# Kernel optimization log

Measured on AMD Instinct MI355X. Metric: run time of the kernel, lower is better.

The kernel has to match this reference:

```python
import jax, jax.numpy as jnp
import numpy as np

B, T, E, H = 32, 256, 1024, 1024


def setup_inputs() -> dict:
    key = jax.random.key(0)
    ks = jax.random.split(key, 8)
    stdv = 1.0 / np.sqrt(H)
    u = lambda k, shape: jax.random.uniform(k, shape, jnp.float32, -stdv, stdv)
    return {
        "x": jax.random.normal(ks[0], (B, T, E), jnp.float32),
        "mask": jnp.ones((B, T), jnp.float32),
        "W_ih0": u(ks[1], (E, 4 * H)),
        "W_hh0": u(ks[2], (H, 4 * H)),
        "b0": jnp.zeros((4 * H,), jnp.float32),
        "W_ih1": u(ks[3], (H, 4 * H)),
        "W_hh1": u(ks[4], (H, 4 * H)),
        "b1": jnp.zeros((4 * H,), jnp.float32),
    }


def _cell(inp, m_t, h0, c0, Wih, Whh, b):
    # pre-activations: [B, 4H]; gate order f, i, o, g (as in torch.split)
    pre = inp @ Wih + h0 @ Whh + b
    f, i, o, g = jnp.split(pre, 4, axis=1)
    m = m_t[:, None]
    c1 = jax.nn.sigmoid(f) * c0 + jax.nn.sigmoid(i) * jnp.tanh(g)
    c1 = c1 * m + c0 * (1.0 - m)
    h1 = jax.nn.sigmoid(o) * jnp.tanh(c1)
    h1 = h1 * m + h0 * (1.0 - m)
    return h1, c1


def reference(x, mask, W_ih0, W_hh0, b0, W_ih1, W_hh1, b1):
    Bz = x.shape[0]
    Hd = W_hh0.shape[0]

    def step(carry, xm):
        h0, c0, h1, c1 = carry
        xt, mt = xm
        # NOTE: layer 1 consumes PREVIOUS timestep's layer-0 hidden (source quirk)
        nh1, nc1 = _cell(h0, mt, h1, c1, W_ih1, W_hh1, b1)
        nh0, nc0 = _cell(xt, mt, h0, c0, W_ih0, W_hh0, b0)
        return (nh0, nc0, nh1, nc1), nh1

    z = jnp.zeros((Bz, Hd), x.dtype)
    init = (z, z, z, z)
    xs = (jnp.swapaxes(x, 0, 1), jnp.swapaxes(mask, 0, 1))  # [T,B,E], [T,B]
    _, hs = jax.lax.scan(step, init, xs)  # hs: [T, B, H]
    states = jnp.swapaxes(hs, 0, 1)  # [B, T, H]
    return states, mask
```

## Files before the change

kernel.cpp:

```cpp
#include <hip/hip_runtime.h>
#include <hip/hip_bf16.h>
#include <stdint.h>
#include <stddef.h>

#define TT    256
#define NBLK  128

typedef __attribute__((ext_vector_type(8))) short short8;
typedef __attribute__((ext_vector_type(4))) float f32x4;

__device__ __forceinline__ short f2bf(float v) {
  uint32_t u = __builtin_bit_cast(uint32_t, v);
  uint32_t r = (u + 0x7fffu + ((u >> 16) & 1u)) >> 16;
  return (short)r;
}

__device__ __forceinline__ void stage_coh(const short8* g, short8* l) {
  __builtin_amdgcn_global_load_lds(
      (const __attribute__((address_space(1))) void*)g,
      (__attribute__((address_space(3))) void*)l, 16, 0, 17);
}
__device__ __forceinline__ void stage_pln(const short8* g, short8* l) {
  __builtin_amdgcn_global_load_lds(
      (const __attribute__((address_space(1))) void*)g,
      (__attribute__((address_space(3))) void*)l, 16, 0, 0);
}

__global__ void k_init(const float* __restrict__ mask, float* __restrict__ out,
                       uint32_t* __restrict__ z) {
  int tid = blockIdx.x * blockDim.x + threadIdx.x;
  if (tid < 8192) out[8388608 + tid] = mask[tid];
  for (int j = tid; j < 51200; j += 16384) z[j] = 0;
}

__global__ void k_packw(const float* __restrict__ Wih0, const float* __restrict__ Whh0,
                        const float* __restrict__ Wih1, const float* __restrict__ Whh1,
                        short* __restrict__ Bp) {
  int cid = blockIdx.x * blockDim.x + threadIdx.x;
  int l    = cid & 63;
  int f    = (cid >> 6) & 63;
  int wgid = cid >> 12;
  int q  = l >> 4, cc = l & 15;
  int cg = f >> 4, s = f & 15;
  int w    = wgid & 3;
  int blk  = (wgid >> 2) & 63;
  bool p1  = (wgid >= 256);
  int precol = (cc >> 2) * 1024 + blk * 16 + cg * 4 + (cc & 3);
  const float* MA = p1 ? Wih1 : Wih0;
  const float* MB = p1 ? Whh1 : Whh0;
  short8 o;
#pragma unroll
  for (int j = 0; j < 8; ++j) {
    int k = w * 512 + s * 32 + q * 8 + j;
    const float* M = (k < 1024) ? MA : MB;
    o[j] = f2bf(M[(size_t)(k & 1023) * 4096 + precol]);
  }
  ((short8*)Bp)[cid] = o;
}

__global__ void k_packx(const float* __restrict__ x, short* __restrict__ Xb) {
  int tid = blockIdx.x * blockDim.x + threadIdx.x;
  int eg = tid & 127;
  int t  = (tid >> 7) & 255;
  int b  = tid >> 15;
  const float* src = x + ((size_t)(b * 256 + t) * 1024 + eg * 8);
  short8 o;
#pragma unroll
  for (int j = 0; j < 8; ++j) o[j] = f2bf(src[j]);
  ((short8*)Xb)[(t * 128 + eg) * 32 + b] = o;
}

__global__ __launch_bounds__(256, 1) void k_lstm(
    const float* __restrict__ mask, const float* __restrict__ b0,
    const float* __restrict__ b1,   const short* __restrict__ Bp,
    const short* __restrict__ Xb,   short* __restrict__ h0r,
    short* __restrict__ h1b,        float* __restrict__ out,
    uint32_t* bar) {
  __shared__ short8 stg[8192];
  f32x4 (*xch)[4][2][64] = (f32x4 (*)[4][2][64])(void*)stg;
  short* hstage = (short*)(void*)(stg + 2048);

  const int tid  = threadIdx.x;
  const int wv   = tid >> 6;
  const int lane = tid & 63;
  const int quad = lane >> 4;
  const int cc   = lane & 15;
  const int bid  = blockIdx.x;
  const bool is1 = (bid >= 64);
  const int blk  = bid & 63;
  const int wgid = (is1 ? 256 : 0) + blk * 4 + wv;
  const int n0w  = blk * 16 + wv * 4;
  const int hcol = n0w + (cc & 3);
  const int kb0  = (wv & 1) * 64;
  const bool coh = !(!is1 && wv < 2);

  uint32_t* const barL   = bar + (is1 ? 1024 : 0);
  uint32_t* const grpC   = barL + (blk & 7) * 32;
  uint32_t* const mstC   = barL + 256;
  uint32_t* const epoL   = barL + 512;
  uint32_t* const epoO   = bar + (is1 ? 0 : 1024) + 512;

  short8 bfr[64];
  {
    const short8* pB = ((const short8*)Bp) + (size_t)wgid * 4096 + lane;
#pragma unroll
    for (int f = 0; f < 64; ++f) bfr[f] = pB[f * 64];
  }
  const float* bias = is1 ? b1 : b0;
  const float bv = bias[(cc >> 2) * 1024 + n0w + (cc & 3)];

  float cst[8], hst[8];
#pragma unroll
  for (int i = 0; i < 8; ++i) { cst[i] = 0.f; hst[i] = 0.f; }

  const int shuf_base = (lane & 48) | (lane & 3);
  const short8* Xq = (const short8*)Xb;
  const short8* H0 = (const short8*)h0r;
  const short8* H1 = (const short8*)h1b;

  short8* const ldsW = stg + wv * 2048;

  const int tmax = is1 ? TT : (TT - 1);

  for (int t = 0; t < tmax; ++t) {
    const int p  = t & 1;
    const int rs = (t + 127) & 127;

    const short8* pan;
    if (!is1) pan = (wv < 2) ? (Xq + (size_t)t * 4096) : (H0 + (size_t)rs * 4096);
    else      pan = (wv < 2) ? (H0 + (size_t)rs * 4096) : (H1 + p * 4096);

    float mrow[8];
#pragma unroll
    for (int i = 0; i < 8; ++i) {
      int r = ((i >> 2) << 4) + quad * 4 + (i & 3);
      mrow[i] = mask[r * 256 + t];
    }

    {
      const short8* gsrc = pan + kb0 * 32 + lane;
      if (coh) {
#pragma unroll
        for (int i = 0; i < 32; ++i) stage_coh(gsrc + i * 64, ldsW + i * 64);
      } else {
#pragma unroll
        for (int i = 0; i < 32; ++i) stage_pln(gsrc + i * 64, ldsW + i * 64);
      }
      asm volatile("s_waitcnt vmcnt(0)" ::: "memory");
      __builtin_amdgcn_sched_barrier(0);
    }

    f32x4 acc[4][2];
#pragma unroll
    for (int cg = 0; cg < 4; ++cg) { acc[cg][0] = (f32x4)0.f; acc[cg][1] = (f32x4)0.f; }

#pragma unroll
    for (int s = 0; s < 16; ++s) {
      short8 a0 = ldsW[(s * 4 + quad) * 32 + cc];
      short8 a1 = ldsW[(s * 4 + quad) * 32 + cc + 16];
#pragma unroll
      for (int cg = 0; cg < 4; ++cg) {
        acc[cg][0] = __builtin_amdgcn_mfma_f32_16x16x32_bf16(a0, bfr[cg * 16 + s], acc[cg][0], 0, 0, 0);
        acc[cg][1] = __builtin_amdgcn_mfma_f32_16x16x32_bf16(a1, bfr[cg * 16 + s], acc[cg][1], 0, 0, 0);
      }
    }

    __syncthreads();
#pragma unroll
    for (int cg = 0; cg < 4; ++cg) {
      if (cg != wv) {
        (*(xch + wv))[cg][0][lane] = acc[cg][0];
        (*(xch + wv))[cg][1][lane] = acc[cg][1];
      }
    }
    __syncthreads();
    f32x4 s0 = acc[wv][0], s1 = acc[wv][1];
#pragma unroll
    for (int w2 = 0; w2 < 4; ++w2) {
      if (w2 != wv) {
        s0 += (*(xch + w2))[wv][0][lane];
        s1 += (*(xch + w2))[wv][1][lane];
      }
    }

    float pv[8];
    pv[0] = s0.x + bv; pv[1] = s0.y + bv; pv[2] = s0.z + bv; pv[3] = s0.w + bv;
    pv[4] = s1.x + bv; pv[5] = s1.y + bv; pv[6] = s1.z + bv; pv[7] = s1.w + bv;

#pragma unroll
    for (int i = 0; i < 8; ++i) {
      float v = pv[i];
      float fg = __shfl(v, shuf_base + 0, 64);
      float ig = __shfl(v, shuf_base + 4, 64);
      float og = __shfl(v, shuf_base + 8, 64);
      float gg = __shfl(v, shuf_base + 12, 64);
      int r = ((i >> 2) << 4) + quad * 4 + (i & 3);
      float m  = mrow[i];
      float om = 1.f - m;
      float sf = 1.f / (1.f + __expf(-fg));
      float si = 1.f / (1.f + __expf(-ig));
      float so = 1.f / (1.f + __expf(-og));
      float e2 = __expf(-2.f * fabsf(gg));
      float tg = (1.f - e2) / (1.f + e2);
      tg = (gg < 0.f) ? -tg : tg;
      float c1 = sf * cst[i] + si * tg;
      c1 = c1 * m + cst[i] * om;
      float ec = __expf(-2.f * fabsf(c1));
      float tc = (1.f - ec) / (1.f + ec);
      tc = (c1 < 0.f) ? -tc : tc;
      float h1 = so * tc;
      h1 = h1 * m + hst[i] * om;
      cst[i] = c1; hst[i] = h1;
      if ((lane & 12) == 0) {
        int hl = wv * 4 + (cc & 3);
        hstage[(hl >> 3) * 256 + r * 8 + (hl & 7)] = f2bf(h1);
        if (is1) out[((size_t)r * 256 + t) * 1024 + hcol] = h1;
      }
    }

    if (is1 && t == TT - 1) break;

    __syncthreads();
    if (wv == 0) {
      short* dst = (is1 ? (h1b + (1 - p) * 32768)
                        : (h0r + (t & 127) * 32768)) + blk * 512 + lane * 8;
      short8 hv = ((const short8*)hstage)[lane];
      asm volatile("global_store_dwordx4 %0, %1, off sc0 sc1"
                   :: "v"(dst), "v"(hv) : "memory");
    }

    if (tid == 0) {
      asm volatile("s_waitcnt vmcnt(0)" ::: "memory");
      uint32_t old = __hip_atomic_fetch_add(grpC, 1u,
                                            __ATOMIC_RELAXED, __HIP_MEMORY_SCOPE_AGENT);
      if ((old & 7) == 7) {
        uint32_t mo = __hip_atomic_fetch_add(mstC, 1u,
                                             __ATOMIC_RELAXED, __HIP_MEMORY_SCOPE_AGENT);
        if ((mo & 7) == 7)
          __hip_atomic_store(epoL, (uint32_t)(t + 1),
                             __ATOMIC_RELAXED, __HIP_MEMORY_SCOPE_AGENT);
      }
      if (t + 1 < tmax) {
        const uint32_t need = (uint32_t)(t + 1);
        if (is1) {
          for (;;) {
            uint32_t eL = __hip_atomic_load(epoL, __ATOMIC_RELAXED, __HIP_MEMORY_SCOPE_AGENT);
            uint32_t eO = __hip_atomic_load(epoO, __ATOMIC_RELAXED, __HIP_MEMORY_SCOPE_AGENT);
            if (eL >= need && eO >= need) break;
            __builtin_amdgcn_s_sleep(2);
          }
        } else if (t >= 127) {
          const uint32_t needO = (uint32_t)(t - 125);
          for (;;) {
            uint32_t eL = __hip_atomic_load(epoL, __ATOMIC_RELAXED, __HIP_MEMORY_SCOPE_AGENT);
            uint32_t eO = __hip_atomic_load(epoO, __ATOMIC_RELAXED, __HIP_MEMORY_SCOPE_AGENT);
            if (eL >= need && eO >= needO) break;
            __builtin_amdgcn_s_sleep(2);
          }
        } else {
          while (__hip_atomic_load(epoL, __ATOMIC_RELAXED, __HIP_MEMORY_SCOPE_AGENT) < need)
            __builtin_amdgcn_s_sleep(2);
        }
      }
    }
    __syncthreads();
  }
}

extern "C" void kernel_launch(void* const* d_in, const int* in_sizes, int n_in,
                              void* d_out, int out_size, void* d_ws, size_t ws_size,
                              hipStream_t stream) {
  const float* x    = (const float*)d_in[0];
  const float* mask = (const float*)d_in[1];
  const float* Wih0 = (const float*)d_in[2];
  const float* Whh0 = (const float*)d_in[3];
  const float* b0   = (const float*)d_in[4];
  const float* Wih1 = (const float*)d_in[5];
  const float* Whh1 = (const float*)d_in[6];
  const float* b1   = (const float*)d_in[7];
  float* out = (float*)d_out;

  char* ws = (char*)d_ws;
  short*    Bp  = (short*)ws;
  short*    Xb  = (short*)(ws + 33554432);
  short*    h0r = (short*)(ws + 50331648);
  short*    h1b = (short*)(ws + 58720256);
  uint32_t* bar = (uint32_t*)(ws + 58851328);
  uint32_t* z   = (uint32_t*)(ws + 58654720);

  hipLaunchKernelGGL(k_init,  dim3(64),   dim3(256), 0, stream, mask, out, z);
  hipLaunchKernelGGL(k_packw, dim3(8192), dim3(256), 0, stream, Wih0, Whh0, Wih1, Whh1, Bp);
  hipLaunchKernelGGL(k_packx, dim3(4096), dim3(256), 0, stream, x, Xb);
  hipLaunchKernelGGL(k_lstm,  dim3(NBLK), dim3(256), 0, stream,
                     mask, b0, b1, Bp, Xb, h0r, h1b, out, bar);
}
```

Baseline: 2.511 ms.

## Replace hierarchical epoch barrier with per-wave spinning on 16 arrival counters

Drops the two-level group/master counter barrier that ended every timestep with a block-wide wait. Each block now bumps one of 16 padded arrival counters after storing its hidden slice. Only the waves that read another block's hidden state spin, and they check all 16 counters in parallel with a wave-wide vote before staging. The cross-wave reduction buffer and hstage get their own LDS arrays, which removes a __syncthreads so the next step's staging can overlap with other waves. This trades a serialized atomic chain for more concurrent polling traffic and relies on the new counters and targets staying consistent with the ring-buffer indexing.

```diff
diff --git a/kernel.cpp b/kernel.cpp
--- a/kernel.cpp
+++ b/kernel.cpp
@@ -24,6 +24,18 @@
   __builtin_amdgcn_global_load_lds(
       (const __attribute__((address_space(1))) void*)g,
       (__attribute__((address_space(3))) void*)l, 16, 0, 0);
+}
+
+__device__ __forceinline__ void spin_lines(const uint32_t* baseA, uint32_t tgtA,
+                                           const uint32_t* baseB, uint32_t tgtB,
+                                           int lane) {
+  const uint32_t* p = (lane < 32 ? baseA : baseB) + (lane & 15) * 32;
+  const uint32_t tgt = (lane < 32) ? tgtA : tgtB;
+  for (;;) {
+    uint32_t v = __hip_atomic_load(p, __ATOMIC_RELAXED, __HIP_MEMORY_SCOPE_AGENT);
+    if (__all(v >= tgt)) break;
+    __builtin_amdgcn_s_sleep(1);
+  }
 }
 
 __global__ void k_init(const float* __restrict__ mask, float* __restrict__ out,
@@ -77,8 +89,8 @@
     short* __restrict__ h1b,        float* __restrict__ out,
     uint32_t* bar) {
   __shared__ short8 stg[8192];
-  f32x4 (*xch)[4][2][64] = (f32x4 (*)[4][2][64])(void*)stg;
-  short* hstage = (short*)(void*)(stg + 2048);
+  __shared__ f32x4 xch[4][3][2][64];
+  __shared__ short hstage[512];
 
   const int tid  = threadIdx.x;
   const int wv   = tid >> 6;
@@ -94,11 +106,9 @@
   const int kb0  = (wv & 1) * 64;
   const bool coh = !(!is1 && wv < 2);
 
-  uint32_t* const barL   = bar + (is1 ? 1024 : 0);
-  uint32_t* const grpC   = barL + (blk & 7) * 32;
-  uint32_t* const mstC   = barL + 256;
-  uint32_t* const epoL   = barL + 512;
-  uint32_t* const epoO   = bar + (is1 ? 0 : 1024) + 512;
+  uint32_t* const lines0 = bar;
+  uint32_t* const lines1 = bar + 1024;
+  uint32_t* const arrC   = (is1 ? lines1 : lines0) + (blk & 15) * 32;
 
   short8 bfr[64];
   {
@@ -137,6 +147,19 @@
       mrow[i] = mask[r * 256 + t];
     }
 
+    if (t > 0) {
+      const uint32_t tgt = (uint32_t)(4 * t);
+      if (!is1) {
+        if (wv >= 2) {
+          uint32_t tgtB = (t >= 127) ? (uint32_t)(4 * (t - 126)) : 0u;
+          spin_lines(lines0, tgt, lines1, tgtB, lane);
+        }
+      } else {
+        if (wv < 2) spin_lines(lines0, tgt, lines0, tgt, lane);
+        else        spin_lines(lines1, tgt, lines1, tgt, lane);
+      }
+    }
+
     {
       const short8* gsrc = pan + kb0 * 32 + lane;
       if (coh) {
@@ -165,12 +188,12 @@
       }
     }
 
-    __syncthreads();
 #pragma unroll
     for (int cg = 0; cg < 4; ++cg) {
       if (cg != wv) {
-        (*(xch + wv))[cg][0][lane] = acc[cg][0];
-        (*(xch + wv))[cg][1][lane] = acc[cg][1];
+        int slot = cg < wv ? cg : cg - 1;
+        xch[wv][slot][0][lane] = acc[cg][0];
+        xch[wv][slot][1][lane] = acc[cg][1];
       }
     }
     __syncthreads();
@@ -178,8 +201,9 @@
 #pragma unroll
     for (int w2 = 0; w2 < 4; ++w2) {
       if (w2 != wv) {
-        s0 += (*(xch + w2))[wv][0][lane];
-        s1 += (*(xch + w2))[wv][1][lane];
+        int slot = wv < w2 ? wv : wv - 1;
+        s0 += xch[w2][slot][0][lane];
+        s1 += xch[w2][slot][1][lane];
       }
     }
 
@@ -227,43 +251,11 @@
       short8 hv = ((const short8*)hstage)[lane];
       asm volatile("global_store_dwordx4 %0, %1, off sc0 sc1"
                    :: "v"(dst), "v"(hv) : "memory");
-    }
-
-    if (tid == 0) {
-      asm volatile("s_waitcnt vmcnt(0)" ::: "memory");
-      uint32_t old = __hip_atomic_fetch_add(grpC, 1u,
-                                            __ATOMIC_RELAXED, __HIP_MEMORY_SCOPE_AGENT);
-      if ((old & 7) == 7) {
-        uint32_t mo = __hip_atomic_fetch_add(mstC, 1u,
-                                             __ATOMIC_RELAXED, __HIP_MEMORY_SCOPE_AGENT);
-        if ((mo & 7) == 7)
-          __hip_atomic_store(epoL, (uint32_t)(t + 1),
-                             __ATOMIC_RELAXED, __HIP_MEMORY_SCOPE_AGENT);
-      }
-      if (t + 1 < tmax) {
-        const uint32_t need = (uint32_t)(t + 1);
-        if (is1) {
-          for (;;) {
-            uint32_t eL = __hip_atomic_load(epoL, __ATOMIC_RELAXED, __HIP_MEMORY_SCOPE_AGENT);
-            uint32_t eO = __hip_atomic_load(epoO, __ATOMIC_RELAXED, __HIP_MEMORY_SCOPE_AGENT);
-            if (eL >= need && eO >= need) break;
-            __builtin_amdgcn_s_sleep(2);
-          }
-        } else if (t >= 127) {
-          const uint32_t needO = (uint32_t)(t - 125);
-          for (;;) {
-            uint32_t eL = __hip_atomic_load(epoL, __ATOMIC_RELAXED, __HIP_MEMORY_SCOPE_AGENT);
-            uint32_t eO = __hip_atomic_load(epoO, __ATOMIC_RELAXED, __HIP_MEMORY_SCOPE_AGENT);
-            if (eL >= need && eO >= needO) break;
-            __builtin_amdgcn_s_sleep(2);
-          }
-        } else {
-          while (__hip_atomic_load(epoL, __ATOMIC_RELAXED, __HIP_MEMORY_SCOPE_AGENT) < need)
-            __builtin_amdgcn_s_sleep(2);
-        }
-      }
-    }
-    __syncthreads();
+      if (lane == 0) {
+        asm volatile("s_waitcnt vmcnt(0)" ::: "memory");
+        __hip_atomic_fetch_add(arrC, 1u, __ATOMIC_RELAXED, __HIP_MEMORY_SCOPE_AGENT);
+      }
+    }
   }
 }
 
```

Measured after the change: 2.555 ms. Within noise of the previous version (+1.8%).
